# Kernel tuning notes

Measured on AMD Instinct MI355X. Metric: run time of the kernel, lower is better.

The kernel has to match this reference:

```python
import jax, jax.numpy as jnp
import numpy as np

PRIME = 2147483647  # 2^31 - 1, MinHash modulus
GAMMA = 0.3
NUM_HEADS = 8


def minhash_sketch(ids, a, b):
    # ids: (B, L, S) int64 atom ids; a,b: (K,) hash coefficients
    # h[b,l,s,k] = (a[k]*id + b[k]) mod PRIME ; signature = min over the set axis S
    h = (ids[..., None] * a + b) % PRIME          # (B, L, S, K)
    return h.min(axis=2)                          # (B, L, K)


def jaccard_from_signatures(sig_q, sig_k):
    # sig_q: (B, Lq, K), sig_k: (B, Lk, K) -> (B, Lq, Lk) fraction of matching slots.
    # Scan over the K hash slots to avoid materializing a (B,Lq,Lk,K) tensor.
    B, Lq, K = sig_q.shape
    Lk = sig_k.shape[1]

    def step(acc, cols):
        qc, kc = cols                              # (B,Lq), (B,Lk)
        return acc + (qc[:, :, None] == kc[:, None, :]).astype(jnp.float32), None

    init = jnp.zeros((B, Lq, Lk), jnp.float32)
    xs = (jnp.moveaxis(sig_q, -1, 0), jnp.moveaxis(sig_k, -1, 0))
    acc, _ = jax.lax.scan(step, init, xs)
    return acc / K


def symdiff_from_jaccard(jacc, size_q, size_k):
    # |A ∩ B| = J/(1+J) * (|A|+|B|)  =>  |A Δ B| = (|A|+|B|) * (1-J)/(1+J)
    tot = size_q[:, :, None] + size_k[:, None, :]   # (B, Lq, Lk)
    return tot * (1.0 - jacc) / (1.0 + jacc)


def setup_inputs() -> dict:
    key = jax.random.key(0)
    ks = jax.random.split(key, 12)
    B, Lq, Lk, E, S, K, V = 4, 1024, 1024, 512, 8, 128, 32000
    w = lambda k: (jax.random.normal(k, (E, E), jnp.float32) * 0.02)
    return {
        "query": jax.random.normal(ks[0], (B, Lq, E), jnp.float32),
        "key": jax.random.normal(ks[1], (B, Lk, E), jnp.float32),
        "value": jax.random.normal(ks[2], (B, Lk, E), jnp.float32),
        "token_sets_q": jax.random.randint(ks[3], (B, Lq, S), 0, V).astype(jnp.int64),
        "token_sets_k": jax.random.randint(ks[4], (B, Lk, S), 0, V).astype(jnp.int64),
        "hash_a": jax.random.randint(ks[5], (K,), 1, PRIME - 1).astype(jnp.int64),
        "hash_b": jax.random.randint(ks[6], (K,), 0, PRIME - 1).astype(jnp.int64),
        "Wq": w(ks[7]), "bq": jnp.zeros((E,), jnp.float32),
        "Wk": w(ks[8]), "bk": jnp.zeros((E,), jnp.float32),
        "Wv": w(ks[9]), "bv": jnp.zeros((E,), jnp.float32),
        "Wo": w(ks[10]), "bo": jnp.zeros((E,), jnp.float32),
    }


def reference(query, key, value, token_sets_q, token_sets_k, hash_a, hash_b,
              Wq, bq, Wk, bk, Wv, bv, Wo, bo):
    B, Lq, E = query.shape
    Lk = key.shape[1]
    H = NUM_HEADS
    d = E // H

    # in-projections (torch Linear: x @ W^T + b); q,k are computed but the
    # attention scores come solely from the token-set kernel (gating disabled)
    q = query @ Wq.T + bq
    k = key @ Wk.T + bk
    v = (value @ Wv.T + bv).reshape(B, Lk, H, d).transpose(0, 2, 1, 3)  # (B,H,Lk,d)

    # MinHash sketches of per-token atom sets -> estimated Jaccard -> Δ-RBF score
    sig_q = minhash_sketch(token_sets_q, hash_a, hash_b)   # (B,Lq,K)
    sig_k = minhash_sketch(token_sets_k, hash_a, hash_b)   # (B,Lk,K)
    jacc = jaccard_from_signatures(sig_q, sig_k)           # (B,Lq,Lk)

    S = token_sets_q.shape[-1]
    size_q = jnp.full((B, Lq), S, jnp.float32)             # uniform CSR offsets -> |set| = S
    size_k = jnp.full((B, Lk), S, jnp.float32)
    delta = symdiff_from_jaccard(jacc, size_q, size_k)
    scores = jnp.exp(-GAMMA * delta)                       # (B,Lq,Lk), shared by all heads

    attn = jax.nn.softmax(scores, axis=-1)                 # no masks, no causal, dropout=0
    ctx = jnp.einsum('bqk,bhkd->bqhd', attn, v).reshape(B, Lq, E)
    return ctx @ Wo.T + bo
```

## Files before the change

kernel.cpp:

```cpp
#include <hip/hip_runtime.h>
#include <hip/hip_bf16.h>
#include <stdint.h>

#define PRIME 2147483647u
#define GAMMA 0.3f
#define K_HASH 128
#define S_SET 8
#define NB 4
#define LQ 1024
#define LK 1024
#define EDIM 512

typedef unsigned short ushort_t;
typedef __attribute__((ext_vector_type(8))) short short8;
typedef __attribute__((ext_vector_type(4))) float f32x4;

static __device__ __forceinline__ unsigned short f2bf(float f) {
    unsigned u = __builtin_bit_cast(unsigned, f);
    u += 0x7FFFu + ((u >> 16) & 1u);
    return (unsigned short)(u >> 16);
}

static __device__ __forceinline__ void glds16(const void* g, void* l) {
    __builtin_amdgcn_global_load_lds(
        (const __attribute__((address_space(1))) unsigned int*)g,
        (__attribute__((address_space(3))) unsigned int*)l, 16, 0, 0);
}

#define SWZ(r) ((((r) >> 2) & 3) ^ ((r) & 3))

static __device__ __forceinline__ float score_of(int m) {
    float r = (float)(K_HASH - m) / (float)(K_HASH + m);
    return expf(expf(-GAMMA * (2.0f * S_SET) * r));
}

#define EPI_NONE 3

template<int OUTF32, int MODE>
static __device__ void gemm64_dev(
        const ushort_t* __restrict__ A, const ushort_t* __restrict__ B,
        void* __restrict__ C,
        int lda, int ldb, int ldc, int Kd, int m0, int n0,
        ushort_t* AsBase, ushort_t* BsBase, int tid) {
    ushort_t (*As)[64 * 32] = (ushort_t (*)[64 * 32])AsBase;
    ushort_t (*Bs)[64 * 32] = (ushort_t (*)[64 * 32])BsBase;
    int w = tid >> 6, lane = tid & 63;
    int wm = (w & 1) * 32, wn = (w >> 1) * 32;
    int mrow = lane & 15, kg = lane >> 4;

    int r = tid >> 2, c = (tid & 3) ^ SWZ(r);
    const ushort_t* pa = A + (size_t)(m0 + r) * lda + c * 8;
    const ushort_t* pb = B + (size_t)(n0 + r) * ldb + c * 8;

    int aoff[2], boff[2];
    #pragma unroll
    for (int s = 0; s < 2; s++) {
        int Ra = wm + s * 16 + mrow;
        aoff[s] = Ra * 32 + (kg ^ SWZ(Ra)) * 8;
        int Rb = wn + s * 16 + mrow;
        boff[s] = Rb * 32 + (kg ^ SWZ(Rb)) * 8;
    }

    f32x4 acc[2][2] = {};
    int nK = Kd >> 5;
    glds16(pa, &As[0][tid * 8]);
    glds16(pb, &Bs[0][tid * 8]);
    for (int i = 0; i < nK; i++) {
        __syncthreads();
        int cur = i & 1, nxt = cur ^ 1;
        if (i + 1 < nK) {
            int k0 = (i + 1) << 5;
            glds16(pa + k0, &As[nxt][tid * 8]);
            glds16(pb + k0, &Bs[nxt][tid * 8]);
        }
        short8 af[2], bh[2];
        #pragma unroll
        for (int s = 0; s < 2; s++) {
            af[s] = *(const short8*)&As[cur][aoff[s]];
            bh[s] = *(const short8*)&Bs[cur][boff[s]];
        }
        #pragma unroll
        for (int ii = 0; ii < 2; ii++)
            #pragma unroll
            for (int jj = 0; jj < 2; jj++)
                acc[ii][jj] = __builtin_amdgcn_mfma_f32_16x16x32_bf16(
                                  af[ii], bh[jj], acc[ii][jj], 0, 0, 0);
    }

    int col = lane & 15, rbase = (lane >> 4) * 4;
    #pragma unroll
    for (int ii = 0; ii < 2; ii++) {
        #pragma unroll
        for (int jj = 0; jj < 2; jj++) {
            #pragma unroll
            for (int rr = 0; rr < 4; rr++) {
                int gm = m0 + wm + ii * 16 + rbase + rr;
                int gn = n0 + wn + jj * 16 + col;
                float v = acc[ii][jj][rr];
                size_t cix = (size_t)gm * ldc + gn;
                if (OUTF32) ((float*)C)[cix] = v;
                else        ((ushort_t*)C)[cix] = f2bf(v);
            }
        }
    }
}

#define CVT_N0 (NB * LK * EDIM)
#define CVT_N1 (EDIM * EDIM)
#define CVT_BLOCKS ((CVT_N0 + CVT_N1) / (256 * 8))
#define MZ_BLOCKS 1024
#define SIGT_BLOCKS 128
#define VBS_BLOCKS 16
#define WVT_BLOCKS 64
#define BOB_BLOCKS 2
#define PREP_GRID (CVT_BLOCKS + MZ_BLOCKS + SIGT_BLOCKS + VBS_BLOCKS + WVT_BLOCKS + BOB_BLOCKS)

__global__ __launch_bounds__(256) void prep_kernel(
        const float* __restrict__ value, const float* __restrict__ Wv,
        const float* __restrict__ Wo, const float* __restrict__ bv,
        const float* __restrict__ bo,
        ushort_t* __restrict__ Vb, ushort_t* __restrict__ Wob,
        ushort_t* __restrict__ WvT,
        const int* __restrict__ ts_q, const int* __restrict__ ts_k,
        const int* __restrict__ ha, const int* __restrict__ hb,
        unsigned* __restrict__ sigTq, unsigned* __restrict__ sigTk,
        uint8_t* __restrict__ M, float* __restrict__ vbsum,
        float* __restrict__ bob) {
    __shared__ unsigned tile[128 * 65];
    __shared__ int ids_s[64 * S_SET];
    __shared__ float vs[256];
    int blk = blockIdx.x, tid = threadIdx.x;
    if (blk < CVT_BLOCKS) {
        size_t i = ((size_t)blk * 256 + tid) * 8;
        const float* src; ushort_t* dst; size_t off;
        if (i < CVT_N0) { src = value; dst = Vb;  off = i; }
        else            { src = Wo;    dst = Wob; off = i - CVT_N0; }
        float4 a = *(const float4*)(src + off);
        float4 b = *(const float4*)(src + off + 4);
        ushort4 o0, o1;
        o0.x = f2bf(a.x); o0.y = f2bf(a.y); o0.z = f2bf(a.z); o0.w = f2bf(a.w);
        o1.x = f2bf(b.x); o1.y = f2bf(b.y); o1.z = f2bf(b.z); o1.w = f2bf(b.w);
        *(ushort4*)(dst + off)     = o0;
        *(ushort4*)(dst + off + 4) = o1;
        return;
    }
    if (blk < CVT_BLOCKS + MZ_BLOCKS) {
        size_t off = ((size_t)(blk - CVT_BLOCKS) * 256 + tid) * 16;
        *(int4*)(M + off) = (int4){0, 0, 0, 0};
        return;
    }
    if (blk < CVT_BLOCKS + MZ_BLOCKS + SIGT_BLOCKS) {
        int sb = blk - (CVT_BLOCKS + MZ_BLOCKS);
        int r0 = sb * 64;
        const int* ts = (r0 < NB * LQ) ? ts_q : ts_k;
        unsigned* sigT = (r0 < NB * LQ) ? sigTq : sigTk;
        int base = r0 & (NB * LQ - 1);
        ((int2*)ids_s)[tid] = ((const int2*)(ts + (size_t)base * S_SET))[tid];
        __syncthreads();
        int kt = tid & 127, rt = tid >> 7;
        unsigned long long a  = (unsigned)ha[kt];
        unsigned long long bb = (unsigned)hb[kt];
        for (int r = rt; r < 64; r += 2) {
            unsigned mn = 0xFFFFFFFFu;
            #pragma unroll
            for (int s = 0; s < S_SET; s++) {
                unsigned long long x =
                    a * (unsigned long long)(unsigned)ids_s[r * S_SET + s] + bb;
                x = (x & PRIME) + (x >> 31);
                x = (x & PRIME) + (x >> 31);
                unsigned rr = (unsigned)x;
                if (rr >= PRIME) rr -= PRIME;
                mn = (rr < mn) ? rr : mn;
            }
            tile[kt * 65 + r] = mn;
        }
        __syncthreads();
        #pragma unroll
        for (int ch = 0; ch < 32; ch++) {
            int idx = ch * 256 + tid;
            int k = idx >> 6, r = idx & 63;
            sigT[(size_t)k * (NB * LQ) + base + r] = tile[k * 65 + r];
        }
        return;
    }
    if (blk < CVT_BLOCKS + MZ_BLOCKS + SIGT_BLOCKS + VBS_BLOCKS) {
        int vb = blk - (CVT_BLOCKS + MZ_BLOCKS + SIGT_BLOCKS);
        int b = vb >> 2, ch = vb & 3;
        int e = ch * 128 + (tid & 127), half = tid >> 7;
        const float* vp = value + ((size_t)(b * LK) + half * 512) * EDIM + e;
        float s = 0.f;
        for (int j = 0; j < 512; j++) s += vp[(size_t)j * EDIM];
        vs[tid] = s;
        __syncthreads();
        if (tid < 128) vbsum[b * EDIM + ch * 128 + tid] = vs[tid] + vs[tid + 128];
        return;
    }
    if (blk < CVT_BLOCKS + MZ_BLOCKS + SIGT_BLOCKS + VBS_BLOCKS + WVT_BLOCKS) {
        int wt = blk - (CVT_BLOCKS + MZ_BLOCKS + SIGT_BLOCKS + VBS_BLOCKS);
        int r0 = (wt >> 3) * 64, c0 = (wt & 7) * 64;
        ushort_t (*tt)[65] = (ushort_t (*)[65])tile;
        #pragma unroll
        for (int p = 0; p < 16; p++) {
            int idx = p * 256 + tid, r = idx >> 6, c = idx & 63;
            tt[c][r] = f2bf(Wv[(size_t)(r0 + r) * EDIM + c0 + c]);
        }
        __syncthreads();
        #pragma unroll
        for (int p = 0; p < 16; p++) {
            int idx = p * 256 + tid, r = idx >> 6, c = idx & 63;
            WvT[(size_t)(c0 + r) * EDIM + r0 + c] = tt[r][c];
        }
        return;
    }
    int bb = blk - (CVT_BLOCKS + MZ_BLOCKS + SIGT_BLOCKS + VBS_BLOCKS + WVT_BLOCKS);
    int n = bb * 256 + tid;
    const float* worow = Wo + (size_t)n * EDIM;
    float acc = bo[n];
    for (int e = 0; e < EDIM; e++) acc += bv[e] * worow[e];
    bob[n] = acc;
}

union JSmem {
    struct { unsigned keys[2048]; ushort_t vals[2048]; } j;
    struct { ushort_t As[2][64 * 32]; ushort_t Bs[2][64 * 32]; } g;
};

__global__ __launch_bounds__(256) void joing1_kernel(
        const unsigned* __restrict__ sigTq, const unsigned* __restrict__ sigTk,
        uint8_t* __restrict__ M,
        const ushort_t* __restrict__ Wob, const ushort_t* __restrict__ WvT,
        ushort_t* __restrict__ Wvo,
        const float* __restrict__ vbsum, const float* __restrict__ Wv,
        float* __restrict__ vpsum) {
    __shared__ JSmem sm;
    int blk = blockIdx.x, tid = threadIdx.x;
    if (blk >= 512 + 64) {
        int vb = blk - 576, b = vb >> 1;
        int ep = (vb & 1) * 256 + tid;
        const float* wvrow = Wv + (size_t)ep * EDIM;
        const float* vbs = vbsum + b * EDIM;
        float acc = 0.f;
        for (int e = 0; e < EDIM; e++) acc += vbs[e] * wvrow[e];
        vpsum[b * EDIM + ep] = acc;
        return;
    }
    if (blk >= 512) {
        int t = blk - 512;
        gemm64_dev<0, EPI_NONE>(Wob, WvT, Wvo,
                                EDIM, EDIM, EDIM, EDIM,
                                (t >> 3) * 64, (t & 7) * 64,
                                sm.g.As[0], sm.g.Bs[0], tid);
        return;
    }
    int b = blk >> 7, k = blk & 127;
    const unsigned* kc = sigTk + (size_t)k * (NB * LK) + b * LK;
    const unsigned* qc = sigTq + (size_t)k * (NB * LQ) + b * LQ;
    uint4 kv = ((const uint4*)kc)[tid];
    uint4 qv = ((const uint4*)qc)[tid];
    #pragma unroll
    for (int i = 0; i < 8; i++) sm.j.keys[i * 256 + tid] = 0xFFFFFFFFu;
    __syncthreads();
    unsigned vvv[4] = {kv.x, kv.y, kv.z, kv.w};
    unsigned hh[4]; bool dn[4];
    #pragma unroll
    for (int e = 0; e < 4; e++) { hh[e] = (vvv[e] * 2654435761u) >> 21; dn[e] = false; }
    int rem = 4;
    while (rem) {
        #pragma unroll
        for (int e = 0; e < 4; e++) {
            if (dn[e]) continue;
            unsigned prev = atomicCAS(&sm.j.keys[hh[e]], 0xFFFFFFFFu, vvv[e]);
            if (prev == 0xFFFFFFFFu) {
                sm.j.vals[hh[e]] = (ushort_t)(tid * 4 + e);
                dn[e] = true; rem--;
            } else hh[e] = (hh[e] + 1) & 2047;
        }
    }
    __syncthreads();
    uint8_t* Mb = M + ((size_t)b << 20);
    unsigned qq[4] = {qv.x, qv.y, qv.z, qv.w};
    #pragma unroll
    for (int e = 0; e < 4; e++) { hh[e] = (qq[e] * 2654435761u) >> 21; dn[e] = false; }
    rem = 4;
    while (rem) {
        unsigned kk[4];
        #pragma unroll
        for (int e = 0; e < 4; e++) kk[e] = sm.j.keys[hh[e]];
        #pragma unroll
        for (int e = 0; e < 4; e++) {
            if (dn[e]) continue;
            if (kk[e] == 0xFFFFFFFFu) { dn[e] = true; rem--; }
            else {
                if (kk[e] == qq[e]) {
                    unsigned ix = ((unsigned)(tid * 4 + e) << 10) + sm.j.vals[hh[e]];
                    atomicAdd((unsigned*)(Mb + (ix & ~3u)), 1u << ((ix & 3u) * 8));
                }
                hh[e] = (hh[e] + 1) & 2047;
            }
        }
    }
}

__global__ __launch_bounds__(256) void g2_kernel(
        const ushort_t* __restrict__ Vb, const ushort_t* __restrict__ Wvo,
        ushort_t* __restrict__ W2c,
        const float* __restrict__ vpsum, const float* __restrict__ Wo,
        float* __restrict__ S) {
    __shared__ ushort_t As[2][64 * 32], Bs[2][64 * 32];
    int blk = blockIdx.x, tid = threadIdx.x;
    if (blk >= 512) {
        int sb = blk - 512, b = sb >> 1;
        int n = (sb & 1) * 256 + tid;
        const float* worow = Wo + (size_t)n * EDIM;
        const float* vps = vpsum + b * EDIM;
        float acc = 0.f;
        for (int e = 0; e < EDIM; e++) acc += vps[e] * worow[e];
        S[b * EDIM + n] = acc;
        return;
    }
    gemm64_dev<0, EPI_NONE>(Vb, Wvo, W2c,
                            EDIM, EDIM, EDIM, EDIM,
                            (blk >> 3) * 64, (blk & 7) * 64,
                            As[0], Bs[0], tid);
}

__global__ __launch_bounds__(256) void outk_kernel(
        const uint8_t* __restrict__ M, const ushort_t* __restrict__ W2c,
        const float* __restrict__ S, const float* __restrict__ bob,
        float* __restrict__ out) {
    __shared__ unsigned lj[256];
    __shared__ float lp[256];
    __shared__ unsigned lcnt;
    int row = blockIdx.x, tid = threadIdx.x, b = row >> 10;
    const uint8_t* Mr = M + ((size_t)row << 10);
    float p0 = score_of(0);
    float acc0 = 0.f, acc1 = 0.f, drs = 0.f;
    int n0 = tid * 2;
    for (int c = 0; c < 4; c++) {
        if (tid == 0) lcnt = 0;
        __syncthreads();
        uint8_t m = Mr[c * 256 + tid];
        if (m) {
            unsigned s = atomicAdd(&lcnt, 1u);
            lj[s] = c * 256 + tid;
            lp[s] = score_of((int)m) - p0;
        }
        __syncthreads();
        unsigned cnt = lcnt;
        for (unsigned i = 0; i < cnt; i++) {
            float w = lp[i];
            drs += w;
            const ushort_t* wr = W2c + (((size_t)(b << 10) + lj[i]) << 9);
            unsigned pk = *(const unsigned*)(wr + n0);
            acc0 += w * __builtin_bit_cast(float, pk << 16);
            acc1 += w * __builtin_bit_cast(float, pk & 0xFFFF0000u);
        }
        __syncthreads();
    }
    float rs = 1024.0f * p0 + drs;
    float inv = 1.0f / rs;
    float2 sv = *(const float2*)(S + b * EDIM + n0);
    float2 bb = *(const float2*)(bob + n0);
    float2 o;
    o.x = (p0 * sv.x + acc0) * inv + bb.x;
    o.y = (p0 * sv.y + acc1) * inv + bb.y;
    *(float2*)(out + (size_t)row * EDIM + n0) = o;
}

extern "C" void kernel_launch(void* const* d_in, const int* in_sizes, int n_in,
                              void* d_out, int out_size, void* d_ws, size_t ws_size,
                              hipStream_t stream) {
    const float* value = (const float*)d_in[2];
    const int* tsq = (const int*)d_in[3];
    const int* tsk = (const int*)d_in[4];
    const int* ha  = (const int*)d_in[5];
    const int* hb  = (const int*)d_in[6];
    const float* Wv = (const float*)d_in[11];
    const float* bv = (const float*)d_in[12];
    const float* Wo = (const float*)d_in[13];
    const float* bo = (const float*)d_in[14];
    float* out = (float*)d_out;

    char* ws = (char*)d_ws;
    unsigned* sigTq = (unsigned*)(ws);
    unsigned* sigTk = (unsigned*)(ws + (2ull << 20));
    uint8_t*  M     = (uint8_t*)(ws + (4ull << 20));
    ushort_t* Vb    = (ushort_t*)(ws + (8ull << 20));
    ushort_t* W2c   = (ushort_t*)(ws + (12ull << 20));
    ushort_t* Wob   = (ushort_t*)(ws + (16ull << 20));
    ushort_t* WvT   = (ushort_t*)(ws + (16ull << 20) + (512ull << 10));
    ushort_t* Wvo   = (ushort_t*)(ws + (17ull << 20));
    float* vbsum    = (float*)(ws + (17ull << 20) + (512ull << 10));
    float* vpsum    = (float*)(ws + (17ull << 20) + (520ull << 10));
    float* S        = (float*)(ws + (17ull << 20) + (528ull << 10));
    float* bob      = (float*)(ws + (17ull << 20) + (536ull << 10));

    prep_kernel<<<PREP_GRID, 256, 0, stream>>>(
        value, Wv, Wo, bv, bo, Vb, Wob, WvT,
        tsq, tsk, ha, hb, sigTq, sigTk, M, vbsum, bob);

    joing1_kernel<<<584, 256, 0, stream>>>(
        sigTq, sigTk, M, Wob, WvT, Wvo, vbsum, Wv, vpsum);

    g2_kernel<<<520, 256, 0, stream>>>(Vb, Wvo, W2c, vpsum, Wo, S);

    outk_kernel<<<NB * LQ, 256, 0, stream>>>(M, W2c, S, bob, out);
}
```

Measured before the change: 177.6 us.

## Fuse column-sum S into g2 GEMM epilogue and parallelize bias fold

Removes the separate value column-sum blocks and the two serial matvec chains (vbsum→vpsum→S) by computing S as per-batch column sums of the W2c GEMM output, accumulated with shuffles and atomics in the GEMM epilogue. The bob bias fold moves to warp-parallel reductions at the start of prep, and a block zeroes S before accumulation. The Wvo GEMM blocks are reordered to run first in joing1. This shortens the long-latency serial loops in tail blocks, at the cost of float atomics (non-deterministic summation order) and S being computed from bf16-rounded inputs.

```diff
diff --git a/kernel.cpp b/kernel.cpp
--- a/kernel.cpp
+++ b/kernel.cpp
@@ -34,12 +34,10 @@
     return expf(expf(-GAMMA * (2.0f * S_SET) * r));
 }
 
-#define EPI_NONE 3
-
-template<int OUTF32, int MODE>
+template<int SEPI>
 static __device__ void gemm64_dev(
         const ushort_t* __restrict__ A, const ushort_t* __restrict__ B,
-        void* __restrict__ C,
+        ushort_t* __restrict__ C, float* __restrict__ Sacc,
         int lda, int ldb, int ldc, int Kd, int m0, int n0,
         ushort_t* AsBase, ushort_t* BsBase, int tid) {
     ushort_t (*As)[64 * 32] = (ushort_t (*)[64 * 32])AsBase;
@@ -96,24 +94,35 @@
             for (int rr = 0; rr < 4; rr++) {
                 int gm = m0 + wm + ii * 16 + rbase + rr;
                 int gn = n0 + wn + jj * 16 + col;
-                float v = acc[ii][jj][rr];
-                size_t cix = (size_t)gm * ldc + gn;
-                if (OUTF32) ((float*)C)[cix] = v;
-                else        ((ushort_t*)C)[cix] = f2bf(v);
+                C[(size_t)gm * ldc + gn] = f2bf(acc[ii][jj][rr]);
             }
         }
     }
-}
-
+    if (SEPI) {
+        #pragma unroll
+        for (int jj = 0; jj < 2; jj++) {
+            float s = 0.f;
+            #pragma unroll
+            for (int ii = 0; ii < 2; ii++)
+                #pragma unroll
+                for (int rr = 0; rr < 4; rr++) s += acc[ii][jj][rr];
+            s += __shfl_xor(s, 16);
+            s += __shfl_xor(s, 32);
+            if ((lane >> 4) == 0)
+                atomicAdd(&Sacc[(m0 >> 10) * EDIM + n0 + wn + jj * 16 + col], s);
+        }
+    }
+}
+
+#define BOB_BLOCKS 8
+#define SZ_BLOCKS 1
 #define CVT_N0 (NB * LK * EDIM)
 #define CVT_N1 (EDIM * EDIM)
 #define CVT_BLOCKS ((CVT_N0 + CVT_N1) / (256 * 8))
 #define MZ_BLOCKS 1024
 #define SIGT_BLOCKS 128
-#define VBS_BLOCKS 16
 #define WVT_BLOCKS 64
-#define BOB_BLOCKS 2
-#define PREP_GRID (CVT_BLOCKS + MZ_BLOCKS + SIGT_BLOCKS + VBS_BLOCKS + WVT_BLOCKS + BOB_BLOCKS)
+#define PREP_GRID (BOB_BLOCKS + SZ_BLOCKS + CVT_BLOCKS + MZ_BLOCKS + SIGT_BLOCKS + WVT_BLOCKS)
 
 __global__ __launch_bounds__(256) void prep_kernel(
         const float* __restrict__ value, const float* __restrict__ Wv,
@@ -124,14 +133,36 @@
         const int* __restrict__ ts_q, const int* __restrict__ ts_k,
         const int* __restrict__ ha, const int* __restrict__ hb,
         unsigned* __restrict__ sigTq, unsigned* __restrict__ sigTk,
-        uint8_t* __restrict__ M, float* __restrict__ vbsum,
+        uint8_t* __restrict__ M, float* __restrict__ S,
         float* __restrict__ bob) {
     __shared__ unsigned tile[128 * 65];
     __shared__ int ids_s[64 * S_SET];
-    __shared__ float vs[256];
     int blk = blockIdx.x, tid = threadIdx.x;
-    if (blk < CVT_BLOCKS) {
-        size_t i = ((size_t)blk * 256 + tid) * 8;
+    if (blk < BOB_BLOCKS) {
+        int w = tid >> 6, lane = tid & 63;
+        #pragma unroll
+        for (int i = 0; i < 16; i++) {
+            int row = blk * 64 + w * 16 + i;
+            const float* wr = Wo + (size_t)row * EDIM;
+            float s = 0.f;
+            #pragma unroll
+            for (int c2 = 0; c2 < 8; c2++)
+                s += bv[lane + 64 * c2] * wr[lane + 64 * c2];
+            #pragma unroll
+            for (int off = 32; off; off >>= 1) s += __shfl_down(s, off);
+            if (lane == 0) bob[row] = bo[row] + s;
+        }
+        return;
+    }
+    if (blk < BOB_BLOCKS + SZ_BLOCKS) {
+        ((float2*)S)[tid] = (float2){0.f, 0.f};
+        ((float2*)S)[256 + tid] = (float2){0.f, 0.f};
+        ((float2*)S)[512 + tid] = (float2){0.f, 0.f};
+        ((float2*)S)[768 + tid] = (float2){0.f, 0.f};
+        return;
+    }
+    if (blk < BOB_BLOCKS + SZ_BLOCKS + CVT_BLOCKS) {
+        size_t i = ((size_t)(blk - BOB_BLOCKS - SZ_BLOCKS) * 256 + tid) * 8;
         const float* src; ushort_t* dst; size_t off;
         if (i < CVT_N0) { src = value; dst = Vb;  off = i; }
         else            { src = Wo;    dst = Wob; off = i - CVT_N0; }
@@ -144,13 +175,13 @@
         *(ushort4*)(dst + off + 4) = o1;
         return;
     }
-    if (blk < CVT_BLOCKS + MZ_BLOCKS) {
-        size_t off = ((size_t)(blk - CVT_BLOCKS) * 256 + tid) * 16;
+    if (blk < BOB_BLOCKS + SZ_BLOCKS + CVT_BLOCKS + MZ_BLOCKS) {
+        size_t off = ((size_t)(blk - BOB_BLOCKS - SZ_BLOCKS - CVT_BLOCKS) * 256 + tid) * 16;
         *(int4*)(M + off) = (int4){0, 0, 0, 0};
         return;
     }
-    if (blk < CVT_BLOCKS + MZ_BLOCKS + SIGT_BLOCKS) {
-        int sb = blk - (CVT_BLOCKS + MZ_BLOCKS);
+    if (blk < BOB_BLOCKS + SZ_BLOCKS + CVT_BLOCKS + MZ_BLOCKS + SIGT_BLOCKS) {
+        int sb = blk - (BOB_BLOCKS + SZ_BLOCKS + CVT_BLOCKS + MZ_BLOCKS);
         int r0 = sb * 64;
         const int* ts = (r0 < NB * LQ) ? ts_q : ts_k;
         unsigned* sigT = (r0 < NB * LQ) ? sigTq : sigTk;
@@ -183,41 +214,20 @@
         }
         return;
     }
-    if (blk < CVT_BLOCKS + MZ_BLOCKS + SIGT_BLOCKS + VBS_BLOCKS) {
-        int vb = blk - (CVT_BLOCKS + MZ_BLOCKS + SIGT_BLOCKS);
-        int b = vb >> 2, ch = vb & 3;
-        int e = ch * 128 + (tid & 127), half = tid >> 7;
-        const float* vp = value + ((size_t)(b * LK) + half * 512) * EDIM + e;
-        float s = 0.f;
-        for (int j = 0; j < 512; j++) s += vp[(size_t)j * EDIM];
-        vs[tid] = s;
-        __syncthreads();
-        if (tid < 128) vbsum[b * EDIM + ch * 128 + tid] = vs[tid] + vs[tid + 128];
-        return;
-    }
-    if (blk < CVT_BLOCKS + MZ_BLOCKS + SIGT_BLOCKS + VBS_BLOCKS + WVT_BLOCKS) {
-        int wt = blk - (CVT_BLOCKS + MZ_BLOCKS + SIGT_BLOCKS + VBS_BLOCKS);
-        int r0 = (wt >> 3) * 64, c0 = (wt & 7) * 64;
-        ushort_t (*tt)[65] = (ushort_t (*)[65])tile;
-        #pragma unroll
-        for (int p = 0; p < 16; p++) {
-            int idx = p * 256 + tid, r = idx >> 6, c = idx & 63;
-            tt[c][r] = f2bf(Wv[(size_t)(r0 + r) * EDIM + c0 + c]);
-        }
-        __syncthreads();
-        #pragma unroll
-        for (int p = 0; p < 16; p++) {
-            int idx = p * 256 + tid, r = idx >> 6, c = idx & 63;
-            WvT[(size_t)(c0 + r) * EDIM + r0 + c] = tt[r][c];
-        }
-        return;
-    }
-    int bb = blk - (CVT_BLOCKS + MZ_BLOCKS + SIGT_BLOCKS + VBS_BLOCKS + WVT_BLOCKS);
-    int n = bb * 256 + tid;
-    const float* worow = Wo + (size_t)n * EDIM;
-    float acc = bo[n];
-    for (int e = 0; e < EDIM; e++) acc += bv[e] * worow[e];
-    bob[n] = acc;
+    int wt = blk - (BOB_BLOCKS + SZ_BLOCKS + CVT_BLOCKS + MZ_BLOCKS + SIGT_BLOCKS);
+    int r0 = (wt >> 3) * 64, c0 = (wt & 7) * 64;
+    ushort_t (*tt)[65] = (ushort_t (*)[65])tile;
+    #pragma unroll
+    for (int p = 0; p < 16; p++) {
+        int idx = p * 256 + tid, r = idx >> 6, c = idx & 63;
+        tt[c][r] = f2bf(Wv[(size_t)(r0 + r) * EDIM + c0 + c]);
+    }
+    __syncthreads();
+    #pragma unroll
+    for (int p = 0; p < 16; p++) {
+        int idx = p * 256 + tid, r = idx >> 6, c = idx & 63;
+        WvT[(size_t)(c0 + r) * EDIM + r0 + c] = tt[r][c];
+    }
 }
 
 union JSmem {
@@ -229,30 +239,17 @@
         const unsigned* __restrict__ sigTq, const unsigned* __restrict__ sigTk,
         uint8_t* __restrict__ M,
         const ushort_t* __restrict__ Wob, const ushort_t* __restrict__ WvT,
-        ushort_t* __restrict__ Wvo,
-        const float* __restrict__ vbsum, const float* __restrict__ Wv,
-        float* __restrict__ vpsum) {
+        ushort_t* __restrict__ Wvo) {
     __shared__ JSmem sm;
     int blk = blockIdx.x, tid = threadIdx.x;
-    if (blk >= 512 + 64) {
-        int vb = blk - 576, b = vb >> 1;
-        int ep = (vb & 1) * 256 + tid;
-        const float* wvrow = Wv + (size_t)ep * EDIM;
-        const float* vbs = vbsum + b * EDIM;
-        float acc = 0.f;
-        for (int e = 0; e < EDIM; e++) acc += vbs[e] * wvrow[e];
-        vpsum[b * EDIM + ep] = acc;
-        return;
-    }
-    if (blk >= 512) {
-        int t = blk - 512;
-        gemm64_dev<0, EPI_NONE>(Wob, WvT, Wvo,
-                                EDIM, EDIM, EDIM, EDIM,
-                                (t >> 3) * 64, (t & 7) * 64,
-                                sm.g.As[0], sm.g.Bs[0], tid);
-        return;
-    }
-    int b = blk >> 7, k = blk & 127;
+    if (blk < 64) {
+        gemm64_dev<0>(Wob, WvT, Wvo, nullptr,
+                      EDIM, EDIM, EDIM, EDIM,
+                      (blk >> 3) * 64, (blk & 7) * 64,
+                      sm.g.As[0], sm.g.Bs[0], tid);
+        return;
+    }
+    int jt = blk - 64, b = jt >> 7, k = jt & 127;
     const unsigned* kc = sigTk + (size_t)k * (NB * LK) + b * LK;
     const unsigned* qc = sigTq + (size_t)k * (NB * LQ) + b * LQ;
     uint4 kv = ((const uint4*)kc)[tid];
@@ -303,25 +300,13 @@
 
 __global__ __launch_bounds__(256) void g2_kernel(
         const ushort_t* __restrict__ Vb, const ushort_t* __restrict__ Wvo,
-        ushort_t* __restrict__ W2c,
-        const float* __restrict__ vpsum, const float* __restrict__ Wo,
-        float* __restrict__ S) {
+        ushort_t* __restrict__ W2c, float* __restrict__ S) {
     __shared__ ushort_t As[2][64 * 32], Bs[2][64 * 32];
-    int blk = blockIdx.x, tid = threadIdx.x;
-    if (blk >= 512) {
-        int sb = blk - 512, b = sb >> 1;
-        int n = (sb & 1) * 256 + tid;
-        const float* worow = Wo + (size_t)n * EDIM;
-        const float* vps = vpsum + b * EDIM;
-        float acc = 0.f;
-        for (int e = 0; e < EDIM; e++) acc += vps[e] * worow[e];
-        S[b * EDIM + n] = acc;
-        return;
-    }
-    gemm64_dev<0, EPI_NONE>(Vb, Wvo, W2c,
-                            EDIM, EDIM, EDIM, EDIM,
-                            (blk >> 3) * 64, (blk & 7) * 64,
-                            As[0], Bs[0], tid);
+    int blk = blockIdx.x;
+    gemm64_dev<1>(Vb, Wvo, W2c, S,
+                  EDIM, EDIM, EDIM, EDIM,
+                  (blk >> 3) * 64, (blk & 7) * 64,
+                  As[0], Bs[0], threadIdx.x);
 }
 
 __global__ __launch_bounds__(256) void outk_kernel(
@@ -390,19 +375,17 @@
     ushort_t* Wob   = (ushort_t*)(ws + (16ull << 20));
     ushort_t* WvT   = (ushort_t*)(ws + (16ull << 20) + (512ull << 10));
     ushort_t* Wvo   = (ushort_t*)(ws + (17ull << 20));
-    float* vbsum    = (float*)(ws + (17ull << 20) + (512ull << 10));
-    float* vpsum    = (float*)(ws + (17ull << 20) + (520ull << 10));
-    float* S        = (float*)(ws + (17ull << 20) + (528ull << 10));
-    float* bob      = (float*)(ws + (17ull << 20) + (536ull << 10));
+    float* S        = (float*)(ws + (17ull << 20) + (512ull << 10));
+    float* bob      = (float*)(ws + (17ull << 20) + (520ull << 10));
 
     prep_kernel<<<PREP_GRID, 256, 0, stream>>>(
         value, Wv, Wo, bv, bo, Vb, Wob, WvT,
-        tsq, tsk, ha, hb, sigTq, sigTk, M, vbsum, bob);
-
-    joing1_kernel<<<584, 256, 0, stream>>>(
-        sigTq, sigTk, M, Wob, WvT, Wvo, vbsum, Wv, vpsum);
-
-    g2_kernel<<<520, 256, 0, stream>>>(Vb, Wvo, W2c, vpsum, Wo, S);
+        tsq, tsk, ha, hb, sigTq, sigTk, M, S, bob);
+
+    joing1_kernel<<<576, 256, 0, stream>>>(
+        sigTq, sigTk, M, Wob, WvT, Wvo);
+
+    g2_kernel<<<512, 256, 0, stream>>>(Vb, Wvo, W2c, S);
 
     outk_kernel<<<NB * LQ, 256, 0, stream>>>(M, W2c, S, bob, out);
 }
```

Result: faster. 161.2 us (-9.2%).
